# Kernel optimization log

Hardware: AMD Instinct MI355X
Metric: run time of the kernel (lower is better)

## Reference

```python
import jax, jax.numpy as jnp
import numpy as np

B, S, H = 32, 2048, 1024

def setup_inputs() -> dict:
    key = jax.random.key(0)
    k1, k2, k3, k4 = jax.random.split(key, 4)
    encoded_states = jax.random.normal(k1, (B, S, H), dtype=jnp.float32)
    # exactly one formula token (label 2) per sample at position 0.
    raw = jax.random.randint(k2, (B, S), 0, 10)
    sr_label = jnp.where(raw < 2, raw, -100)
    sr_label = sr_label.at[:, 0].set(2)
    W1 = jax.random.normal(k3, (H, 2 * H), dtype=jnp.float32) * (1.0 / np.sqrt(2 * H))
    b1 = jnp.zeros((H,), dtype=jnp.float32)
    W2 = jax.random.normal(k4, (2, H), dtype=jnp.float32) * (1.0 / np.sqrt(H))
    b2 = jnp.zeros((2,), dtype=jnp.float32)
    return {"encoded_states": encoded_states, "sr_label": sr_label,
            "W1": W1, "b1": b1, "W2": W2, "b2": b2}

def reference(encoded_states, sr_label, W1, b1, W2, b2):
    dt = encoded_states.dtype
    header_mask = (sr_label >= 0) & (sr_label < 2)          # (b, s)
    formula_mask = (sr_label == 2).astype(dt)               # exactly one per row
    # gather the single formula embedding per sample via masked sum
    formula_emb = jnp.einsum('bs,bsh->bh', formula_mask, encoded_states)  # (b, h)
    fuse = jnp.concatenate(
        [encoded_states, jnp.broadcast_to(formula_emb[:, None, :], encoded_states.shape)],
        axis=-1)                                             # (b, s, 2h)
    hid = jax.nn.gelu(jnp.einsum('bsf,hf->bsh', fuse, W1) + b1, approximate=False)
    logits = jnp.einsum('bsh,ch->bsc', hid, W2) + b2         # (b, s, 2)
    logp = jax.nn.log_softmax(logits, axis=-1)
    labels = jnp.clip(sr_label, 0, 1)                        # safe index; masked below
    tok_loss = -jnp.take_along_axis(logp, labels[..., None], axis=-1)[..., 0]
    m = header_mask.astype(dt)
    cnt = m.sum(axis=1)                                      # valid headers per sample
    sample_loss = (tok_loss * m).sum(axis=1) / jnp.maximum(cnt, 1.0)  # CE mean per sample
    valid = (cnt > 0).astype(dt)
    loss = (sample_loss * valid).sum() / (valid.sum() + 1e-6)
    return loss, logits, header_mask
```

## Files before the change

kernel.cpp:

```cpp
#include <hip/hip_runtime.h>
#include <math.h>


typedef __bf16 bf16x8 __attribute__((ext_vector_type(8)));
typedef float f32x4 __attribute__((ext_vector_type(4)));

struct alignas(16) BF8 { __bf16 h[8]; };
struct alignas(8)  BF4 { __bf16 h[4]; };

typedef const __attribute__((address_space(1))) void glb_void;
typedef __attribute__((address_space(3))) void lds_void;

#define SEQ 2048
#define NB  32
#define HID 1024
#define MROWS (NB * SEQ)
#define NKT 16

__device__ __forceinline__ float gelu_bf(float x) {
    float z  = 0.70710678118f * x;
    float az = fabsf(z);
    float t  = __builtin_amdgcn_rcpf(fmaf(0.3275911f, az, 1.0f));
    float poly = fmaf(fmaf(fmaf(fmaf(1.061405429f, t, -1.453152027f), t,
                         1.421413741f), t, -0.284496736f), t, 0.254829592f) * t;
    float ex = __expf(-az * az);
    float er = copysignf(fmaf(-poly, ex, 1.0f), z);
    return 0.5f * x * (1.0f + er);
}

__global__ void sr_init_logits(float* __restrict__ logits, const float* __restrict__ b2) {
    int i = blockIdx.x * 256 + threadIdx.x;
    if (i < MROWS * 2) logits[i] = b2[i & 1];
}

__global__ void sr_conv_w1(const float* __restrict__ W1, __bf16* __restrict__ Bt) {
    int gid = blockIdx.x * 256 + threadIdx.x;
    int h = gid >> 8;
    int kb = (gid & 255) * 4;
    float4 v = *(const float4*)&W1[(size_t)h * 2048 + kb];
    BF4 o;
    o.h[0] = (__bf16)v.x; o.h[1] = (__bf16)v.y; o.h[2] = (__bf16)v.z; o.h[3] = (__bf16)v.w;
    *(BF4*)&Bt[(size_t)h * 1024 + kb] = o;
}

__global__ void sr_conv_enc(const float* __restrict__ enc, __bf16* __restrict__ Ab) {
    size_t i = ((size_t)blockIdx.x * 256 + threadIdx.x) * 8;
    float4 v0 = *(const float4*)&enc[i];
    float4 v1 = *(const float4*)&enc[i + 4];
    BF8 t;
    t.h[0] = (__bf16)v0.x; t.h[1] = (__bf16)v0.y;
    t.h[2] = (__bf16)v0.z; t.h[3] = (__bf16)v0.w;
    t.h[4] = (__bf16)v1.x; t.h[5] = (__bf16)v1.y;
    t.h[6] = (__bf16)v1.z; t.h[7] = (__bf16)v1.w;
    *(BF8*)&Ab[i] = t;
}

__global__ void sr_femb(const float* __restrict__ enc, const int* __restrict__ lab,
                        float* __restrict__ femb) {
    __shared__ int cnt;
    __shared__ int idl[64];
    int b = blockIdx.x;
    int tid = threadIdx.x;
    if (tid == 0) cnt = 0;
    __syncthreads();
    for (int s = tid; s < SEQ; s += 256)
        if (lab[b * SEQ + s] == 2) {
            int p = atomicAdd(&cnt, 1);
            if (p < 64) idl[p] = s;
        }
    __syncthreads();
    float4 a = {0.f, 0.f, 0.f, 0.f};
    int n = cnt < 64 ? cnt : 64;
    for (int i = 0; i < n; ++i) {
        float4 v = *(const float4*)&enc[((size_t)b * SEQ + idl[i]) * HID + tid * 4];
        a.x += v.x; a.y += v.y; a.z += v.z; a.w += v.w;
    }
    *(float4*)&femb[b * HID + tid * 4] = a;
}

__global__ void sr_fc(const float* __restrict__ femb, const float* __restrict__ W1,
                      const float* __restrict__ b1, float* __restrict__ fcout) {
    int gw = (blockIdx.x * 256 + threadIdx.x) >> 6;
    int lane = threadIdx.x & 63;
    for (int i = 0; i < 16; ++i) {
        int d = gw * 16 + i;
        int b = d >> 10, h = d & 1023;
        const float* fe = femb + b * HID;
        const float* wr = W1 + (size_t)h * 2048 + 1024;
        float p = 0.f;
        #pragma unroll
        for (int t = 0; t < 16; ++t) {
            int k = lane + t * 64;
            p += fe[k] * wr[k];
        }
        #pragma unroll
        for (int off = 32; off; off >>= 1) p += __shfl_down(p, off);
        if (lane == 0) fcout[d] = p + b1[h];
    }
}

__global__ __launch_bounds__(512, 2)
void sr_gemm9(const __bf16* __restrict__ Ab, const __bf16* __restrict__ Bt,
              const float* __restrict__ fc, const float* __restrict__ W2,
              float* __restrict__ partg) {
    __shared__ __align__(16) unsigned char smem[139264];
    __bf16* LAb = (__bf16*)smem;
    __bf16* LBb = (__bf16*)(smem + 65536);
    float*  red = (float*)smem;

    int bid = blockIdx.x;
    int lgc = (bid & 7) * 128 + (bid >> 3);
    int pm = lgc >> 2, pn = lgc & 3;
    const int row0 = pm * 256, col0 = pn * 256;

    int tid = threadIdx.x;
    int wid = tid >> 6, lane = tid & 63;
    int wr = wid >> 2, wc = wid & 3;
    int l15 = lane & 15, lq = lane >> 4;

    f32x4 acc[2][2][4][2] = {};

    #define STAGE(buf, kt) do {                                                   \
        _Pragma("unroll")                                                         \
        for (int i = 0; i < 4; ++i) {                                             \
            int q = i * 512 + tid;                                                \
            int r = q >> 3, c = q & 7;                                            \
            int sc = (c ^ (r & 7)) * 8 + (kt) * 64;                               \
            __builtin_amdgcn_global_load_lds(                                     \
                (glb_void*)(Ab + (size_t)(row0 + r) * HID + sc),                  \
                (lds_void*)(LAb + (buf) * 16384 + q * 8), 16, 0, 0);              \
            __builtin_amdgcn_global_load_lds(                                     \
                (glb_void*)(Bt + (size_t)(col0 + r) * HID + sc),                  \
                (lds_void*)(LBb + (buf) * 16384 + q * 8), 16, 0, 0);              \
        }                                                                         \
    } while (0)

    STAGE(0, 0);
    __syncthreads();

    int cur = 0;
    for (int kt = 0; kt < NKT; ++kt) {
        if (kt + 1 < NKT) STAGE(cur ^ 1, kt + 1);

        const __bf16* LAc = LAb + cur * 16384;
        const __bf16* LBc = LBb + cur * 16384;
        bf16x8 bfr[2][2][2];
        #pragma unroll
        for (int qb = 0; qb < 2; ++qb)
            #pragma unroll
            for (int n = 0; n < 2; ++n)
                #pragma unroll
                for (int kk = 0; kk < 2; ++kk) {
                    int r = qb * 128 + wc * 32 + n * 16 + l15;
                    bfr[qb][n][kk] = *(const bf16x8*)
                        &LBc[r * 64 + (((kk * 4 + lq) ^ (r & 7)) * 8)];
                }
        #pragma unroll
        for (int qa = 0; qa < 2; ++qa) {
            bf16x8 af[4][2];
            #pragma unroll
            for (int m = 0; m < 4; ++m)
                #pragma unroll
                for (int kk = 0; kk < 2; ++kk) {
                    int r = qa * 128 + wr * 64 + m * 16 + l15;
                    af[m][kk] = *(const bf16x8*)
                        &LAc[r * 64 + (((kk * 4 + lq) ^ (r & 7)) * 8)];
                }
            #pragma unroll
            for (int qb = 0; qb < 2; ++qb)
                #pragma unroll
                for (int m = 0; m < 4; ++m)
                    #pragma unroll
                    for (int n = 0; n < 2; ++n)
                        #pragma unroll
                        for (int kk = 0; kk < 2; ++kk)
                            acc[qa][qb][m][n] = __builtin_amdgcn_mfma_f32_16x16x32_bf16(
                                af[m][kk], bfr[qb][n][kk], acc[qa][qb][m][n], 0, 0, 0);
        }
        __syncthreads();
        cur ^= 1;
    }
    #undef STAGE

    int b = row0 >> 11;
    float fcv[2][2], w2a[2][2], w2b[2][2];
    #pragma unroll
    for (int qb = 0; qb < 2; ++qb)
        #pragma unroll
        for (int n = 0; n < 2; ++n) {
            int h = col0 + qb * 128 + wc * 32 + n * 16 + l15;
            fcv[qb][n] = fc[b * HID + h];
            w2a[qb][n] = W2[h];
            w2b[qb][n] = W2[HID + h];
        }
    int e = wc * 16 + l15;
    #pragma unroll
    for (int qa = 0; qa < 2; ++qa)
        #pragma unroll
        for (int m = 0; m < 4; ++m)
            #pragma unroll
            for (int j = 0; j < 4; ++j) {
                int rloc = qa * 128 + wr * 64 + m * 16 + lq * 4 + j;
                float p0 = 0.f, p1 = 0.f;
                #pragma unroll
                for (int qb = 0; qb < 2; ++qb)
                    #pragma unroll
                    for (int n = 0; n < 2; ++n) {
                        float g = gelu_bf(acc[qa][qb][m][n][j] + fcv[qb][n]);
                        p0 += g * w2a[qb][n];
                        p1 += g * w2b[qb][n];
                    }
                red[(rloc * 2 + 0) * 68 + e] = p0;
                red[(rloc * 2 + 1) * 68 + e] = p1;
            }
    __syncthreads();
    {
        const f32x4* rp = (const f32x4*)&red[tid * 68];
        f32x4 sv = {0.f, 0.f, 0.f, 0.f};
        #pragma unroll
        for (int i = 0; i < 16; ++i) sv += rp[i];
        float s = sv[0] + sv[1] + sv[2] + sv[3];
        int row = tid >> 1, c = tid & 1;
        partg[((size_t)pn * MROWS + row0 + row) * 2 + c] = s;
    }
}

__global__ __launch_bounds__(256, 2)
void sr_gemm_fused(const float* __restrict__ enc, const __bf16* __restrict__ Bt,
                   const float* __restrict__ fc, const float* __restrict__ W2,
                   float* __restrict__ logits) {
    __shared__ __bf16 As[128 * 64];
    __shared__ __bf16 Bs[128 * 64];

    int bid = blockIdx.x;
    int logical = (bid & 7) * 512 + (bid >> 3);
    int pm = logical >> 3;
    int pn = logical & 7;

    int tid = threadIdx.x;
    int wid = tid >> 6, lane = tid & 63;
    int wm = wid >> 1, wn = wid & 1;

    const int row0 = pm * 128;
    const int col0 = pn * 128;

    f32x4 acc[4][4] = {};

    for (int kt = 0; kt < 16; ++kt) {
        int k0 = kt * 64;
        #pragma unroll
        for (int i = 0; i < 4; ++i) {
            int q = i * 256 + tid;
            int r = q >> 3;
            int cb = (q & 7) * 8;
            const __bf16* src = Bt + (size_t)(col0 + r) * 1024 + k0 + cb;
            __builtin_amdgcn_global_load_lds((glb_void*)src, (lds_void*)&Bs[q * 8], 16, 0, 0);
        }
        #pragma unroll
        for (int pp = 0; pp < 4; ++pp) {
            int e = pp * 2048 + tid * 8;
            int r = e >> 6, c = e & 63;
            const float* src = enc + (size_t)(row0 + r) * 1024 + k0 + c;
            float4 f0 = *(const float4*)src;
            float4 f1 = *(const float4*)(src + 4);
            BF8 t;
            t.h[0] = (__bf16)f0.x; t.h[1] = (__bf16)f0.y;
            t.h[2] = (__bf16)f0.z; t.h[3] = (__bf16)f0.w;
            t.h[4] = (__bf16)f1.x; t.h[5] = (__bf16)f1.y;
            t.h[6] = (__bf16)f1.z; t.h[7] = (__bf16)f1.w;
            *(BF8*)&As[r * 64 + c] = t;
        }
        __syncthreads();
        int lrow = lane & 15;
        int ak = (lane >> 4) * 8;
        #pragma unroll
        for (int kk = 0; kk < 2; ++kk) {
            bf16x8 a[4], b[4];
            #pragma unroll
            for (int m = 0; m < 4; ++m)
                a[m] = *(const bf16x8*)&As[(wm * 64 + m * 16 + lrow) * 64 + kk * 32 + ak];
            #pragma unroll
            for (int n = 0; n < 4; ++n)
                b[n] = *(const bf16x8*)&Bs[(wn * 64 + n * 16 + lrow) * 64 + kk * 32 + ak];
            #pragma unroll
            for (int m = 0; m < 4; ++m)
                #pragma unroll
                for (int n = 0; n < 4; ++n)
                    acc[m][n] = __builtin_amdgcn_mfma_f32_16x16x32_bf16(a[m], b[n], acc[m][n], 0, 0, 0);
        }
        __syncthreads();
    }

    int bidx = row0 >> 11;
    float fcv[4], w2a[4], w2b[4];
    #pragma unroll
    for (int n = 0; n < 4; ++n) {
        int h = col0 + wn * 64 + n * 16 + (lane & 15);
        fcv[n] = fc[bidx * HID + h];
        w2a[n] = W2[h];
        w2b[n] = W2[HID + h];
    }
    #pragma unroll
    for (int m = 0; m < 4; ++m) {
        int rbase = row0 + wm * 64 + m * 16 + (lane >> 4) * 4;
        #pragma unroll
        for (int j = 0; j < 4; ++j) {
            float p0 = 0.f, p1 = 0.f;
            #pragma unroll
            for (int n = 0; n < 4; ++n) {
                float g = gelu_bf(acc[m][n][j] + fcv[n]);
                p0 += g * w2a[n];
                p1 += g * w2b[n];
            }
            #pragma unroll
            for (int off = 1; off < 16; off <<= 1) {
                p0 += __shfl_xor(p0, off);
                p1 += __shfl_xor(p1, off);
            }
            if ((lane & 15) == 0) {
                int rg = rbase + j;
                atomicAdd(&logits[rg * 2 + 0], p0);
                atomicAdd(&logits[rg * 2 + 1], p1);
            }
        }
    }
}

__global__ void sr_loss_pg(const int* __restrict__ lab, const float* __restrict__ partg,
                           const float* __restrict__ b2, float* __restrict__ logits,
                           float* __restrict__ mask_out, float* __restrict__ sl,
                           float* __restrict__ validv) {
    int b = blockIdx.x;
    int tid = threadIdx.x;
    float b20 = b2[0], b21 = b2[1];
    float lsum = 0.f; int lcnt = 0;
    for (int s = tid; s < SEQ; s += 256) {
        size_t row = (size_t)b * SEQ + s;
        float l0 = b20, l1 = b21;
        #pragma unroll
        for (int q = 0; q < 4; ++q) {
            l0 += partg[((size_t)q * MROWS + row) * 2 + 0];
            l1 += partg[((size_t)q * MROWS + row) * 2 + 1];
        }
        logits[row * 2 + 0] = l0;
        logits[row * 2 + 1] = l1;
        int l = lab[row];
        bool hdr = (l == 0) || (l == 1);
        mask_out[row] = hdr ? 1.0f : 0.0f;
        if (hdr) {
            float mx = fmaxf(l0, l1);
            float lse = mx + logf(expf(l0 - mx) + expf(l1 - mx));
            lsum += lse - (l == 0 ? l0 : l1);
            lcnt++;
        }
    }
    #pragma unroll
    for (int off = 32; off; off >>= 1) {
        lsum += __shfl_down(lsum, off);
        lcnt += __shfl_down(lcnt, off);
    }
    __shared__ float wsum[4];
    __shared__ int wcnt[4];
    int wid = tid >> 6, lane = tid & 63;
    if (lane == 0) { wsum[wid] = lsum; wcnt[wid] = lcnt; }
    __syncthreads();
    if (tid == 0) {
        float S = wsum[0] + wsum[1] + wsum[2] + wsum[3];
        int C = wcnt[0] + wcnt[1] + wcnt[2] + wcnt[3];
        sl[b] = (C > 0) ? S / (float)C : 0.0f;
        validv[b] = (C > 0) ? 1.0f : 0.0f;
    }
}

__global__ void sr_loss(const int* __restrict__ lab, const float* __restrict__ logits,
                        float* __restrict__ mask_out, float* __restrict__ sl,
                        float* __restrict__ validv) {
    int b = blockIdx.x;
    int tid = threadIdx.x;
    float lsum = 0.f; int lcnt = 0;
    for (int s = tid; s < SEQ; s += 256) {
        int l = lab[b * SEQ + s];
        bool hdr = (l == 0) || (l == 1);
        mask_out[b * SEQ + s] = hdr ? 1.0f : 0.0f;
        if (hdr) {
            float l0 = logits[(b * SEQ + s) * 2];
            float l1 = logits[(b * SEQ + s) * 2 + 1];
            float mx = fmaxf(l0, l1);
            float lse = mx + logf(expf(l0 - mx) + expf(l1 - mx));
            lsum += lse - (l == 0 ? l0 : l1);
            lcnt++;
        }
    }
    #pragma unroll
    for (int off = 32; off; off >>= 1) {
        lsum += __shfl_down(lsum, off);
        lcnt += __shfl_down(lcnt, off);
    }
    __shared__ float wsum[4];
    __shared__ int wcnt[4];
    int wid = tid >> 6, lane = tid & 63;
    if (lane == 0) { wsum[wid] = lsum; wcnt[wid] = lcnt; }
    __syncthreads();
    if (tid == 0) {
        float S = wsum[0] + wsum[1] + wsum[2] + wsum[3];
        int C = wcnt[0] + wcnt[1] + wcnt[2] + wcnt[3];
        sl[b] = (C > 0) ? S / (float)C : 0.0f;
        validv[b] = (C > 0) ? 1.0f : 0.0f;
    }
}

__global__ void sr_final(const float* __restrict__ sl, const float* __restrict__ validv,
                         float* __restrict__ out) {
    if (threadIdx.x == 0) {
        float s = 0.f, v = 0.f;
        for (int b = 0; b < NB; ++b) { s += sl[b]; v += validv[b]; }
        out[0] = s / (v + 1e-6f);
    }
}

extern "C" void kernel_launch(void* const* d_in, const int* in_sizes, int n_in,
                              void* d_out, int out_size, void* d_ws, size_t ws_size,
                              hipStream_t stream) {
    const float* enc = (const float*)d_in[0];
    const int*   lab = (const int*)d_in[1];
    const float* W1  = (const float*)d_in[2];
    const float* b1  = (const float*)d_in[3];
    const float* W2  = (const float*)d_in[4];
    const float* b2  = (const float*)d_in[5];

    float* out     = (float*)d_out;
    float* loss    = out;
    float* logits  = out + 1;
    float* maskout = out + 1 + MROWS * 2;

    float* ws     = (float*)d_ws;
    float* femb   = ws;
    float* fc     = ws + 32768;
    float* sl     = ws + 65536;
    float* validv = ws + 65568;
    float* partg  = ws + 65600;
    __bf16* Bt    = (__bf16*)(ws + 65600 + 2 * 524288);
    __bf16* Ab    = Bt + (size_t)HID * HID;

    const size_t need = (65600u + 2u * 524288u) * 4u + (size_t)HID * HID * 2u
                      + (size_t)MROWS * HID * 2u;

    sr_conv_w1<<<1024, 256, 0, stream>>>(W1, Bt);
    sr_femb<<<32, 256, 0, stream>>>(enc, lab, femb);
    sr_fc<<<512, 256, 0, stream>>>(femb, W1, b1, fc);

    if (ws_size >= need) {
        sr_conv_enc<<<32768, 256, 0, stream>>>(enc, Ab);
        sr_gemm9<<<1024, 512, 0, stream>>>(Ab, Bt, fc, W2, partg);
        sr_loss_pg<<<32, 256, 0, stream>>>(lab, partg, b2, logits, maskout, sl, validv);
    } else {
        sr_init_logits<<<512, 256, 0, stream>>>(logits, b2);
        sr_gemm_fused<<<4096, 256, 0, stream>>>(enc, Bt, fc, W2, logits);
        sr_loss<<<32, 256, 0, stream>>>(lab, logits, maskout, sl, validv);
    }

    sr_final<<<1, 64, 0, stream>>>(sl, validv, loss);
}
```

Baseline: 248.8 us.

## Split GEMM main loop into half-tile stages with finer-grained LDS prefetch overlap

Replaces the double-buffered full-tile k-loop with a schedule that splits each 256x256 tile into 128-row halves of A and B. Each half is loaded into its own LDS slot as soon as the previous consumer of that slot is done, interleaved between the four MFMA quadrants. The loop uses explicit barriers, vmcnt/lgkmcnt waits and s_setprio around MFMA blocks, so global-to-LDS loads overlap compute more continuously and fewer loads are in flight at once. The risk is subtle hazards in slot reuse and the hand-tuned wait counts. There is also some redundant loading at the tail, where the k index is clamped to the last tile.

Result: slower. 264.4 us (+6.3%).

```diff
diff --git a/kernel.cpp b/kernel.cpp
--- a/kernel.cpp
+++ b/kernel.cpp
@@ -119,68 +119,118 @@
     int l15 = lane & 15, lq = lane >> 4;
 
     f32x4 acc[2][2][4][2] = {};
-
-    #define STAGE(buf, kt) do {                                                   \
+    bf16x8 af[4][2];
+    bf16x8 bfr[2][2][2];
+
+    #define STG(SRC, ROWB, LBASE, SLOT, KT, HH) do {                              \
         _Pragma("unroll")                                                         \
-        for (int i = 0; i < 4; ++i) {                                             \
+        for (int i = 0; i < 2; ++i) {                                             \
             int q = i * 512 + tid;                                                \
             int r = q >> 3, c = q & 7;                                            \
-            int sc = (c ^ (r & 7)) * 8 + (kt) * 64;                               \
+            int sc = (c ^ (r & 7)) * 8 + (KT) * 64;                               \
             __builtin_amdgcn_global_load_lds(                                     \
-                (glb_void*)(Ab + (size_t)(row0 + r) * HID + sc),                  \
-                (lds_void*)(LAb + (buf) * 16384 + q * 8), 16, 0, 0);              \
-            __builtin_amdgcn_global_load_lds(                                     \
-                (glb_void*)(Bt + (size_t)(col0 + r) * HID + sc),                  \
-                (lds_void*)(LBb + (buf) * 16384 + q * 8), 16, 0, 0);              \
+                (glb_void*)((SRC) + (size_t)((ROWB) + (HH) * 128 + r) * HID + sc),\
+                (lds_void*)((LBASE) + (SLOT) * 8192 + q * 8), 16, 0, 0);          \
         }                                                                         \
     } while (0)
 
-    STAGE(0, 0);
-    __syncthreads();
-
-    int cur = 0;
-    for (int kt = 0; kt < NKT; ++kt) {
-        if (kt + 1 < NKT) STAGE(cur ^ 1, kt + 1);
-
-        const __bf16* LAc = LAb + cur * 16384;
-        const __bf16* LBc = LBb + cur * 16384;
-        bf16x8 bfr[2][2][2];
-        #pragma unroll
-        for (int qb = 0; qb < 2; ++qb)
-            #pragma unroll
-            for (int n = 0; n < 2; ++n)
-                #pragma unroll
-                for (int kk = 0; kk < 2; ++kk) {
-                    int r = qb * 128 + wc * 32 + n * 16 + l15;
-                    bfr[qb][n][kk] = *(const bf16x8*)
-                        &LBc[r * 64 + (((kk * 4 + lq) ^ (r & 7)) * 8)];
-                }
-        #pragma unroll
-        for (int qa = 0; qa < 2; ++qa) {
-            bf16x8 af[4][2];
-            #pragma unroll
-            for (int m = 0; m < 4; ++m)
-                #pragma unroll
-                for (int kk = 0; kk < 2; ++kk) {
-                    int r = qa * 128 + wr * 64 + m * 16 + l15;
-                    af[m][kk] = *(const bf16x8*)
-                        &LAc[r * 64 + (((kk * 4 + lq) ^ (r & 7)) * 8)];
-                }
-            #pragma unroll
-            for (int qb = 0; qb < 2; ++qb)
-                #pragma unroll
-                for (int m = 0; m < 4; ++m)
-                    #pragma unroll
-                    for (int n = 0; n < 2; ++n)
-                        #pragma unroll
-                        for (int kk = 0; kk < 2; ++kk)
-                            acc[qa][qb][m][n] = __builtin_amdgcn_mfma_f32_16x16x32_bf16(
-                                af[m][kk], bfr[qb][n][kk], acc[qa][qb][m][n], 0, 0, 0);
-        }
-        __syncthreads();
-        cur ^= 1;
-    }
-    #undef STAGE
+    #define RD_A(HB)                                                              \
+        _Pragma("unroll") for (int m = 0; m < 4; ++m)                             \
+        _Pragma("unroll") for (int kk = 0; kk < 2; ++kk) {                        \
+            int r = wr * 64 + m * 16 + l15;                                       \
+            af[m][kk] = *(const bf16x8*)&(HB)[r * 64 + (((kk*4+lq) ^ (r&7)) * 8)];\
+        }
+
+    #define RD_B(QB, HB)                                                          \
+        _Pragma("unroll") for (int n = 0; n < 2; ++n)                             \
+        _Pragma("unroll") for (int kk = 0; kk < 2; ++kk) {                        \
+            int r = wc * 32 + n * 16 + l15;                                       \
+            bfr[QB][n][kk] = *(const bf16x8*)&(HB)[r * 64 + (((kk*4+lq) ^ (r&7)) * 8)];\
+        }
+
+    #define MM(QA, QB)                                                            \
+        _Pragma("unroll") for (int m = 0; m < 4; ++m)                             \
+        _Pragma("unroll") for (int n = 0; n < 2; ++n)                             \
+        _Pragma("unroll") for (int kk = 0; kk < 2; ++kk)                          \
+            acc[QA][QB][m][n] = __builtin_amdgcn_mfma_f32_16x16x32_bf16(          \
+                af[m][kk], bfr[QB][n][kk], acc[QA][QB][m][n], 0, 0, 0);
+
+    #define BAR()  __builtin_amdgcn_s_barrier()
+    #define LGKM0() do { asm volatile("s_waitcnt lgkmcnt(0)" ::: "memory");       \
+                         __builtin_amdgcn_sched_barrier(0); } while (0)
+
+    #define KTILE(SA, SNB, K1, K2)                                                \
+    {                                                                             \
+        const __bf16* LA0 = LAb + (SA) * 8192;                                    \
+        const __bf16* LA1 = LA0 + 8192;                                           \
+        const __bf16* LB0 = LBb + (SA) * 8192;                                    \
+        const __bf16* LB1 = LB0 + 8192;                                           \
+                     \
+        RD_A(LA0);                                                                \
+        RD_B(0, LB0);                                                             \
+        STG(Bt, col0, LBb, SNB, K1, 0);                                           \
+        BAR(); LGKM0();                                                           \
+        __builtin_amdgcn_s_setprio(1);                                            \
+        MM(0, 0);                                                                 \
+        __builtin_amdgcn_s_setprio(0);                                            \
+        BAR();                                                                    \
+                            \
+        RD_B(1, LB1);                                                             \
+        STG(Ab, row0, LAb, SA, K2, 0);                                            \
+        BAR(); LGKM0();                                                           \
+        __builtin_amdgcn_s_setprio(1);                                            \
+        MM(0, 1);                                                                 \
+        __builtin_amdgcn_s_setprio(0);                                            \
+        BAR();                                                                    \
+             \
+        RD_A(LA1);                                                                \
+        STG(Bt, col0, LBb, (SA) + 1, K2, 1);                                      \
+        BAR(); LGKM0();                                                           \
+        __builtin_amdgcn_s_setprio(1);                                            \
+        MM(1, 0);                                                                 \
+        __builtin_amdgcn_s_setprio(0);                                            \
+        BAR();                                                                    \
+               \
+        STG(Ab, row0, LAb, (SA) + 1, K2, 1);                                      \
+        BAR();                                                                    \
+        __builtin_amdgcn_s_setprio(1);                                            \
+        MM(1, 1);                                                                 \
+        __builtin_amdgcn_s_setprio(0);                                            \
+        asm volatile("s_waitcnt vmcnt(6)" ::: "memory");                          \
+        __builtin_amdgcn_sched_barrier(0);                                        \
+        BAR();                                                                    \
+    }
+
+    STG(Ab, row0, LAb, 0, 0, 0);
+    STG(Bt, col0, LBb, 0, 0, 0);
+    STG(Bt, col0, LBb, 1, 0, 1);
+    STG(Ab, row0, LAb, 1, 0, 1);
+    STG(Ab, row0, LAb, 2, 1, 0);
+    STG(Bt, col0, LBb, 3, 1, 1);
+    STG(Ab, row0, LAb, 3, 1, 1);
+    asm volatile("s_waitcnt vmcnt(6)" ::: "memory");
+    __builtin_amdgcn_sched_barrier(0);
+    BAR();
+
+    for (int u = 0; u < 8; ++u) {
+        int kt0 = 2 * u, kt1 = 2 * u + 1;
+        int k2a = (kt0 + 2 < NKT) ? kt0 + 2 : NKT - 1;
+        int k2b = (kt1 + 2 < NKT) ? kt1 + 2 : NKT - 1;
+        KTILE(0, 2, kt1, k2a);
+        KTILE(2, 0, k2a, k2b);
+    }
+
+    asm volatile("s_waitcnt vmcnt(0)" ::: "memory");
+    __builtin_amdgcn_sched_barrier(0);
+    BAR();
+
+    #undef KTILE
+    #undef STG
+    #undef RD_A
+    #undef RD_B
+    #undef MM
+    #undef BAR
+    #undef LGKM0
 
     int b = row0 >> 11;
     float fcv[2][2], w2a[2][2], w2b[2][2];
```

## Fuse fp32-to-bf16 conversion of encoder states into the GEMM A-tile load

Applied to the files above, without the earlier changes.

Removes the separate conversion kernel that wrote a bf16 copy of the 256 MB encoder tensor. The GEMM now loads fp32 A tiles into registers for the next k-step, computes on the current buffer, then converts and writes them to LDS before the barrier. This drops one full write and re-read of the bf16 A matrix, but the GEMM reads twice the A bytes per tile (fp32) and loses async global-to-LDS loads for A. Each N-tile block re-reads its fp32 A rows, four times in total, and holding the prefetched values adds register pressure.

Result: slower. 263.2 us (+5.8%).

```diff
diff --git a/kernel.cpp b/kernel.cpp
--- a/kernel.cpp
+++ b/kernel.cpp
@@ -41,18 +41,6 @@
     BF4 o;
     o.h[0] = (__bf16)v.x; o.h[1] = (__bf16)v.y; o.h[2] = (__bf16)v.z; o.h[3] = (__bf16)v.w;
     *(BF4*)&Bt[(size_t)h * 1024 + kb] = o;
-}
-
-__global__ void sr_conv_enc(const float* __restrict__ enc, __bf16* __restrict__ Ab) {
-    size_t i = ((size_t)blockIdx.x * 256 + threadIdx.x) * 8;
-    float4 v0 = *(const float4*)&enc[i];
-    float4 v1 = *(const float4*)&enc[i + 4];
-    BF8 t;
-    t.h[0] = (__bf16)v0.x; t.h[1] = (__bf16)v0.y;
-    t.h[2] = (__bf16)v0.z; t.h[3] = (__bf16)v0.w;
-    t.h[4] = (__bf16)v1.x; t.h[5] = (__bf16)v1.y;
-    t.h[6] = (__bf16)v1.z; t.h[7] = (__bf16)v1.w;
-    *(BF8*)&Ab[i] = t;
 }
 
 __global__ void sr_femb(const float* __restrict__ enc, const int* __restrict__ lab,
@@ -100,9 +88,9 @@
 }
 
 __global__ __launch_bounds__(512, 2)
-void sr_gemm9(const __bf16* __restrict__ Ab, const __bf16* __restrict__ Bt,
-              const float* __restrict__ fc, const float* __restrict__ W2,
-              float* __restrict__ partg) {
+void sr_gemm11(const float* __restrict__ enc, const __bf16* __restrict__ Bt,
+               const float* __restrict__ fc, const float* __restrict__ W2,
+               float* __restrict__ partg) {
     __shared__ __align__(16) unsigned char smem[139264];
     __bf16* LAb = (__bf16*)smem;
     __bf16* LBb = (__bf16*)(smem + 65536);
@@ -119,28 +107,56 @@
     int l15 = lane & 15, lq = lane >> 4;
 
     f32x4 acc[2][2][4][2] = {};
-
-    #define STAGE(buf, kt) do {                                                   \
+    float4 fa[4][2];
+
+    #define LOAD_A(kt) do {                                                       \
+        _Pragma("unroll")                                                         \
+        for (int i = 0; i < 4; ++i) {                                             \
+            int q = i * 512 + tid;                                                \
+            int r = q >> 3, c = q & 7;                                            \
+            int sc = (c ^ (r & 7)) * 8 + (kt) * 64;                               \
+            const float* s0 = &enc[(size_t)(row0 + r) * HID + sc];                \
+            fa[i][0] = *(const float4*)s0;                                        \
+            fa[i][1] = *(const float4*)(s0 + 4);                                  \
+        }                                                                         \
+    } while (0)
+
+    #define WRITE_A(buf) do {                                                     \
+        _Pragma("unroll")                                                         \
+        for (int i = 0; i < 4; ++i) {                                             \
+            int q = i * 512 + tid;                                                \
+            BF8 t;                                                                \
+            t.h[0] = (__bf16)fa[i][0].x; t.h[1] = (__bf16)fa[i][0].y;             \
+            t.h[2] = (__bf16)fa[i][0].z; t.h[3] = (__bf16)fa[i][0].w;             \
+            t.h[4] = (__bf16)fa[i][1].x; t.h[5] = (__bf16)fa[i][1].y;             \
+            t.h[6] = (__bf16)fa[i][1].z; t.h[7] = (__bf16)fa[i][1].w;             \
+            *(BF8*)&LAb[(buf) * 16384 + q * 8] = t;                               \
+        }                                                                         \
+    } while (0)
+
+    #define STAGE_B(buf, kt) do {                                                 \
         _Pragma("unroll")                                                         \
         for (int i = 0; i < 4; ++i) {                                             \
             int q = i * 512 + tid;                                                \
             int r = q >> 3, c = q & 7;                                            \
             int sc = (c ^ (r & 7)) * 8 + (kt) * 64;                               \
             __builtin_amdgcn_global_load_lds(                                     \
-                (glb_void*)(Ab + (size_t)(row0 + r) * HID + sc),                  \
-                (lds_void*)(LAb + (buf) * 16384 + q * 8), 16, 0, 0);              \
-            __builtin_amdgcn_global_load_lds(                                     \
                 (glb_void*)(Bt + (size_t)(col0 + r) * HID + sc),                  \
                 (lds_void*)(LBb + (buf) * 16384 + q * 8), 16, 0, 0);              \
         }                                                                         \
     } while (0)
 
-    STAGE(0, 0);
+    LOAD_A(0);
+    STAGE_B(0, 0);
+    WRITE_A(0);
     __syncthreads();
 
     int cur = 0;
     for (int kt = 0; kt < NKT; ++kt) {
-        if (kt + 1 < NKT) STAGE(cur ^ 1, kt + 1);
+        if (kt + 1 < NKT) {
+            LOAD_A(kt + 1);
+            STAGE_B(cur ^ 1, kt + 1);
+        }
 
         const __bf16* LAc = LAb + cur * 16384;
         const __bf16* LBc = LBb + cur * 16384;
@@ -177,10 +193,14 @@
                             acc[qa][qb][m][n] = __builtin_amdgcn_mfma_f32_16x16x32_bf16(
                                 af[m][kk], bfr[qb][n][kk], acc[qa][qb][m][n], 0, 0, 0);
         }
+
+        if (kt + 1 < NKT) WRITE_A(cur ^ 1);
         __syncthreads();
         cur ^= 1;
     }
-    #undef STAGE
+    #undef LOAD_A
+    #undef WRITE_A
+    #undef STAGE_B
 
     int b = row0 >> 11;
     float fcv[2][2], w2a[2][2], w2b[2][2];
@@ -440,18 +460,15 @@
     float* validv = ws + 65568;
     float* partg  = ws + 65600;
     __bf16* Bt    = (__bf16*)(ws + 65600 + 2 * 524288);
-    __bf16* Ab    = Bt + (size_t)HID * HID;
-
-    const size_t need = (65600u + 2u * 524288u) * 4u + (size_t)HID * HID * 2u
-                      + (size_t)MROWS * HID * 2u;
+
+    const size_t need = (65600u + 2u * 524288u) * 4u + (size_t)HID * HID * 2u;
 
     sr_conv_w1<<<1024, 256, 0, stream>>>(W1, Bt);
     sr_femb<<<32, 256, 0, stream>>>(enc, lab, femb);
     sr_fc<<<512, 256, 0, stream>>>(femb, W1, b1, fc);
 
     if (ws_size >= need) {
-        sr_conv_enc<<<32768, 256, 0, stream>>>(enc, Ab);
-        sr_gemm9<<<1024, 512, 0, stream>>>(Ab, Bt, fc, W2, partg);
+        sr_gemm11<<<1024, 512, 0, stream>>>(enc, Bt, fc, W2, partg);
         sr_loss_pg<<<32, 256, 0, stream>>>(lab, partg, b2, logits, maskout, sl, validv);
     } else {
         sr_init_logits<<<512, 256, 0, stream>>>(logits, b2);
```

## Double GEMM block to 1024 threads with smaller per-warp tile

Applied to the files above, without the earlier changes.

The fused bf16 GEMM kernel now runs 1024 threads (16 waves) per 256x256 block instead of 512. Each wave computes a 64x64 sub-tile with 16 accumulators instead of 32, and the staging loop and final row reduction are split across twice as many threads, the reduction using a shuffle. The aim is more waves to hide LDS and MFMA latency and lower register pressure per thread. In exchange, B fragments are reread from LDS by more waves, and a 139KB shared buffer still limits how many blocks fit per CU.

Measured after the change: 254.9 us. 2.4% more time.

```diff
diff --git a/kernel.cpp b/kernel.cpp
--- a/kernel.cpp
+++ b/kernel.cpp
@@ -99,10 +99,10 @@
     }
 }
 
-__global__ __launch_bounds__(512, 2)
-void sr_gemm9(const __bf16* __restrict__ Ab, const __bf16* __restrict__ Bt,
-              const float* __restrict__ fc, const float* __restrict__ W2,
-              float* __restrict__ partg) {
+__global__ __launch_bounds__(1024, 4)
+void sr_gemm14(const __bf16* __restrict__ Ab, const __bf16* __restrict__ Bt,
+               const float* __restrict__ fc, const float* __restrict__ W2,
+               float* __restrict__ partg) {
     __shared__ __align__(16) unsigned char smem[139264];
     __bf16* LAb = (__bf16*)smem;
     __bf16* LBb = (__bf16*)(smem + 65536);
@@ -118,12 +118,12 @@
     int wr = wid >> 2, wc = wid & 3;
     int l15 = lane & 15, lq = lane >> 4;
 
-    f32x4 acc[2][2][4][2] = {};
+    f32x4 acc[4][4] = {};
 
     #define STAGE(buf, kt) do {                                                   \
         _Pragma("unroll")                                                         \
-        for (int i = 0; i < 4; ++i) {                                             \
-            int q = i * 512 + tid;                                                \
+        for (int i = 0; i < 2; ++i) {                                             \
+            int q = i * 1024 + tid;                                               \
             int r = q >> 3, c = q & 7;                                            \
             int sc = (c ^ (r & 7)) * 8 + (kt) * 64;                               \
             __builtin_amdgcn_global_load_lds(                                     \
@@ -144,38 +144,30 @@
 
         const __bf16* LAc = LAb + cur * 16384;
         const __bf16* LBc = LBb + cur * 16384;
-        bf16x8 bfr[2][2][2];
-        #pragma unroll
-        for (int qb = 0; qb < 2; ++qb)
-            #pragma unroll
-            for (int n = 0; n < 2; ++n)
+        bf16x8 bfr[4][2];
+        #pragma unroll
+        for (int n = 0; n < 4; ++n)
+            #pragma unroll
+            for (int kk = 0; kk < 2; ++kk) {
+                int r = wc * 64 + n * 16 + l15;
+                bfr[n][kk] = *(const bf16x8*)
+                    &LBc[r * 64 + (((kk * 4 + lq) ^ (r & 7)) * 8)];
+            }
+        #pragma unroll
+        for (int m = 0; m < 4; ++m) {
+            bf16x8 af[2];
+            #pragma unroll
+            for (int kk = 0; kk < 2; ++kk) {
+                int r = wr * 64 + m * 16 + l15;
+                af[kk] = *(const bf16x8*)
+                    &LAc[r * 64 + (((kk * 4 + lq) ^ (r & 7)) * 8)];
+            }
+            #pragma unroll
+            for (int n = 0; n < 4; ++n)
                 #pragma unroll
-                for (int kk = 0; kk < 2; ++kk) {
-                    int r = qb * 128 + wc * 32 + n * 16 + l15;
-                    bfr[qb][n][kk] = *(const bf16x8*)
-                        &LBc[r * 64 + (((kk * 4 + lq) ^ (r & 7)) * 8)];
-                }
-        #pragma unroll
-        for (int qa = 0; qa < 2; ++qa) {
-            bf16x8 af[4][2];
-            #pragma unroll
-            for (int m = 0; m < 4; ++m)
-                #pragma unroll
-                for (int kk = 0; kk < 2; ++kk) {
-                    int r = qa * 128 + wr * 64 + m * 16 + l15;
-                    af[m][kk] = *(const bf16x8*)
-                        &LAc[r * 64 + (((kk * 4 + lq) ^ (r & 7)) * 8)];
-                }
-            #pragma unroll
-            for (int qb = 0; qb < 2; ++qb)
-                #pragma unroll
-                for (int m = 0; m < 4; ++m)
-                    #pragma unroll
-                    for (int n = 0; n < 2; ++n)
-                        #pragma unroll
-                        for (int kk = 0; kk < 2; ++kk)
-                            acc[qa][qb][m][n] = __builtin_amdgcn_mfma_f32_16x16x32_bf16(
-                                af[m][kk], bfr[qb][n][kk], acc[qa][qb][m][n], 0, 0, 0);
+                for (int kk = 0; kk < 2; ++kk)
+                    acc[m][n] = __builtin_amdgcn_mfma_f32_16x16x32_bf16(
+                        af[kk], bfr[n][kk], acc[m][n], 0, 0, 0);
         }
         __syncthreads();
         cur ^= 1;
@@ -183,45 +175,43 @@
     #undef STAGE
 
     int b = row0 >> 11;
-    float fcv[2][2], w2a[2][2], w2b[2][2];
-    #pragma unroll
-    for (int qb = 0; qb < 2; ++qb)
-        #pragma unroll
-        for (int n = 0; n < 2; ++n) {
-            int h = col0 + qb * 128 + wc * 32 + n * 16 + l15;
-            fcv[qb][n] = fc[b * HID + h];
-            w2a[qb][n] = W2[h];
-            w2b[qb][n] = W2[HID + h];
-        }
+    float fcv[4], w2a[4], w2b[4];
+    #pragma unroll
+    for (int n = 0; n < 4; ++n) {
+        int h = col0 + wc * 64 + n * 16 + l15;
+        fcv[n] = fc[b * HID + h];
+        w2a[n] = W2[h];
+        w2b[n] = W2[HID + h];
+    }
     int e = wc * 16 + l15;
     #pragma unroll
-    for (int qa = 0; qa < 2; ++qa)
-        #pragma unroll
-        for (int m = 0; m < 4; ++m)
-            #pragma unroll
-            for (int j = 0; j < 4; ++j) {
-                int rloc = qa * 128 + wr * 64 + m * 16 + lq * 4 + j;
-                float p0 = 0.f, p1 = 0.f;
-                #pragma unroll
-                for (int qb = 0; qb < 2; ++qb)
-                    #pragma unroll
-                    for (int n = 0; n < 2; ++n) {
-                        float g = gelu_bf(acc[qa][qb][m][n][j] + fcv[qb][n]);
-                        p0 += g * w2a[qb][n];
-                        p1 += g * w2b[qb][n];
-                    }
-                red[(rloc * 2 + 0) * 68 + e] = p0;
-                red[(rloc * 2 + 1) * 68 + e] = p1;
-            }
+    for (int m = 0; m < 4; ++m)
+        #pragma unroll
+        for (int j = 0; j < 4; ++j) {
+            int rloc = wr * 64 + m * 16 + lq * 4 + j;
+            float p0 = 0.f, p1 = 0.f;
+            #pragma unroll
+            for (int n = 0; n < 4; ++n) {
+                float g = gelu_bf(acc[m][n][j] + fcv[n]);
+                p0 += g * w2a[n];
+                p1 += g * w2b[n];
+            }
+            red[(rloc * 2 + 0) * 68 + e] = p0;
+            red[(rloc * 2 + 1) * 68 + e] = p1;
+        }
     __syncthreads();
     {
-        const f32x4* rp = (const f32x4*)&red[tid * 68];
+        int rc = tid >> 1, half = tid & 1;
+        const f32x4* rp = (const f32x4*)&red[rc * 68 + half * 32];
         f32x4 sv = {0.f, 0.f, 0.f, 0.f};
         #pragma unroll
-        for (int i = 0; i < 16; ++i) sv += rp[i];
+        for (int i = 0; i < 8; ++i) sv += rp[i];
         float s = sv[0] + sv[1] + sv[2] + sv[3];
-        int row = tid >> 1, c = tid & 1;
-        partg[((size_t)pn * MROWS + row0 + row) * 2 + c] = s;
+        s += __shfl_xor(s, 1);
+        if (half == 0) {
+            int row = rc >> 1, c = rc & 1;
+            partg[((size_t)pn * MROWS + row0 + row) * 2 + c] = s;
+        }
     }
 }
 
@@ -451,7 +441,7 @@
 
     if (ws_size >= need) {
         sr_conv_enc<<<32768, 256, 0, stream>>>(enc, Ab);
-        sr_gemm9<<<1024, 512, 0, stream>>>(Ab, Bt, fc, W2, partg);
+        sr_gemm14<<<1024, 1024, 0, stream>>>(Ab, Bt, fc, W2, partg);
         sr_loss_pg<<<32, 256, 0, stream>>>(lab, partg, b2, logits, maskout, sl, validv);
     } else {
         sr_init_logits<<<512, 256, 0, stream>>>(logits, b2);
```
